# Kernel tuning notes

Hardware: AMD Instinct MI355X
Metric: run time of the kernel (lower is better)

Reference implementation:

```python
import jax, jax.numpy as jnp
import numpy as np

D_MODEL = 1024
NUM_HEADS = 16
HEAD_DIM = D_MODEL // NUM_HEADS


def setup_inputs() -> dict:
    key = jax.random.key(0)
    ks = jax.random.split(key, 9)
    B, S = 4, 2048
    s = 1.0 / np.sqrt(D_MODEL)
    return {
        "x": jax.random.normal(ks[0], (B, S, D_MODEL), dtype=jnp.float32),
        "Wq": jax.random.normal(ks[1], (D_MODEL, D_MODEL), dtype=jnp.float32) * s,
        "bq": jnp.zeros((D_MODEL,), dtype=jnp.float32),
        "Wk": jax.random.normal(ks[2], (D_MODEL, HEAD_DIM), dtype=jnp.float32) * s,
        "bk": jnp.zeros((HEAD_DIM,), dtype=jnp.float32),
        "Wv": jax.random.normal(ks[3], (D_MODEL, HEAD_DIM), dtype=jnp.float32) * s,
        "bv": jnp.zeros((HEAD_DIM,), dtype=jnp.float32),
        "Wo": jax.random.normal(ks[4], (D_MODEL, D_MODEL), dtype=jnp.float32) * s,
        "bo": jnp.zeros((D_MODEL,), dtype=jnp.float32),
    }


def reference(x, Wq, bq, Wk, bk, Wv, bv, Wo, bo):
    B, S, _ = x.shape
    H, Dh = NUM_HEADS, HEAD_DIM
    # projections
    Q = (x @ Wq + bq).reshape(B, S, H, Dh).transpose(0, 2, 1, 3)  # [B,H,S,Dh]
    K = x @ Wk + bk  # [B,S,Dh] (single shared KV head)
    V = x @ Wv + bv  # [B,S,Dh]
    # scores: Q @ K^T, broadcasting the single K head over all query heads
    A = jnp.einsum("bhqd,bkd->bhqk", Q, K)  # [B,H,S,S]
    causal = jnp.tril(jnp.ones((S, S), dtype=bool))
    A = jnp.where(causal, A, -jnp.inf)
    # original divides AFTER masking; -inf stays -inf so math is identical
    P = jax.nn.softmax(A / np.sqrt(Dh).astype(np.float32), axis=-1)
    O = jnp.einsum("bhqk,bkd->bhqd", P, V)  # [B,H,S,Dh]
    O = O.transpose(0, 2, 1, 3).reshape(B, S, H * Dh)
    return O @ Wo + bo
```

## Files before the change

kernel.cpp:

```cpp
#include <hip/hip_runtime.h>
#include <hip/hip_bf16.h>

typedef __bf16 bf16_t;
typedef __bf16 bf16x4 __attribute__((ext_vector_type(4)));
typedef __bf16 bf16x8 __attribute__((ext_vector_type(8)));
typedef float f32x4 __attribute__((ext_vector_type(4)));

#define AS1(p) ((const __attribute__((address_space(1))) void*)(p))
#define AS3(p) ((__attribute__((address_space(3))) void*)(p))

__device__ __forceinline__ f32x4 mfma16(bf16x8 a, bf16x8 b, f32x4 c) {
  return __builtin_amdgcn_mfma_f32_16x16x32_bf16(a, b, c, 0, 0, 0);
}

__global__ void prep(const float* __restrict__ x, const float* __restrict__ Wq,
                     const float* __restrict__ Wk, const float* __restrict__ Wv,
                     const float* __restrict__ Wo, const float* __restrict__ bq,
                     const float* __restrict__ bk, const float* __restrict__ bv,
                     bf16_t* __restrict__ xb, bf16_t* __restrict__ WqT,
                     bf16_t* __restrict__ WkvT, bf16_t* __restrict__ WoT,
                     float* __restrict__ bqkv) {
  const int u = blockIdx.x;
  if (u >= 546) {
    int i = ((u - 546) * 256 + threadIdx.x) * 4;
    float4 v = *(const float4*)(x + i);
    bf16x4 o = {(bf16_t)v.x, (bf16_t)v.y, (bf16_t)v.z, (bf16_t)v.w};
    *(bf16x4*)(xb + i) = o;
    return;
  }
  if (u == 544) {
    int i = threadIdx.x * 4;
    *(float4*)(bqkv + i) = *(const float4*)(bq + i);
    return;
  }
  if (u == 545) {
    if (threadIdx.x < 128)
      bqkv[1024 + threadIdx.x] =
          (threadIdx.x < 64) ? bk[threadIdx.x] : bv[threadIdx.x - 64];
    return;
  }
  const float* W; bf16_t* Wt; int N, bx, by;
  if (u < 256)      { W = Wq; Wt = WqT;              N = 1024; bx = u & 15;         by = u >> 4; }
  else if (u < 272) { W = Wk; Wt = WkvT;             N = 64;   bx = 0;              by = u - 256; }
  else if (u < 288) { W = Wv; Wt = WkvT + 64 * 1024; N = 64;   bx = 0;              by = u - 272; }
  else              { W = Wo; Wt = WoT;              N = 1024; bx = (u - 288) & 15; by = (u - 288) >> 4; }
  __shared__ float t[64][65];
  const int n0 = bx * 64, k0 = by * 64;
  const int tx = threadIdx.x & 63, ty = threadIdx.x >> 6;
#pragma unroll
  for (int i = 0; i < 16; ++i)
    t[ty * 16 + i][tx] = W[(size_t)(k0 + ty * 16 + i) * N + n0 + tx];
  __syncthreads();
#pragma unroll
  for (int i = 0; i < 16; ++i)
    Wt[(size_t)(n0 + ty * 16 + i) * 1024 + k0 + tx] = (bf16_t)t[tx][ty * 16 + i];
}

__global__ __launch_bounds__(256, 2)
void gemm_qkv(const bf16_t* __restrict__ A, const bf16_t* __restrict__ Bt,
              const float* __restrict__ bias, bf16_t* __restrict__ Qb,
              bf16_t* __restrict__ KVb, bf16_t* __restrict__ VtG, int M, int K) {
  __shared__ __align__(16) bf16_t As[128 * 32];
  __shared__ __align__(16) bf16_t Bs[128 * 32];
  const int tid = threadIdx.x;
  const int w = tid >> 6, l = tid & 63;
  const int l15 = l & 15, q = l >> 4;
  const int m0 = blockIdx.y * 128, n0 = blockIdx.x * 128;
  const int mw = (w >> 1) * 64, nw = (w & 1) * 64;
  f32x4 acc[4][4] = {};
  const int kb = (l & 3) * 8;
  int rA[2], rB[2];
#pragma unroll
  for (int i = 0; i < 2; ++i) {
    int row = (i * 4 + w) * 16 + (l >> 2);
    rA[i] = m0 + row;
    rB[i] = n0 + row;
  }
  for (int k0 = 0; k0 < K; k0 += 32) {
#pragma unroll
    for (int i = 0; i < 2; ++i) {
      int sg = i * 4 + w;
      __builtin_amdgcn_global_load_lds(AS1(A + (size_t)rA[i] * K + k0 + kb),
                                       AS3(As + sg * 512), 16, 0, 0);
      __builtin_amdgcn_global_load_lds(AS1(Bt + (size_t)rB[i] * K + k0 + kb),
                                       AS3(Bs + sg * 512), 16, 0, 0);
    }
    __syncthreads();
    bf16x8 af[4], bfr[4];
#pragma unroll
    for (int mi = 0; mi < 4; ++mi)
      af[mi] = *(const bf16x8*)(As + (mw + mi * 16 + l15) * 32 + q * 8);
#pragma unroll
    for (int ni = 0; ni < 4; ++ni)
      bfr[ni] = *(const bf16x8*)(Bs + (nw + ni * 16 + l15) * 32 + q * 8);
#pragma unroll
    for (int mi = 0; mi < 4; ++mi)
#pragma unroll
      for (int ni = 0; ni < 4; ++ni)
        acc[mi][ni] = mfma16(af[mi], bfr[ni], acc[mi][ni]);
    __syncthreads();
  }
#pragma unroll
  for (int ni = 0; ni < 4; ++ni) {
    int col = n0 + nw + ni * 16 + l15;
    float bv = bias[col];
#pragma unroll
    for (int mi = 0; mi < 4; ++mi)
#pragma unroll
      for (int r = 0; r < 4; ++r) {
        int row = m0 + mw + mi * 16 + q * 4 + r;
        bf16_t v = (bf16_t)(acc[mi][ni][r] + bv);
        if (col < 1024) {
          Qb[(size_t)row * 1024 + col] = v;
        } else {
          int c2 = col - 1024;
          KVb[(size_t)row * 128 + c2] = v;
          if (c2 >= 64)
            VtG[(size_t)((row >> 11) * 64 + (c2 - 64)) * 2048 + (row & 2047)] = v;
        }
      }
  }
}

__global__ __launch_bounds__(256, 2)
void gemm_nt_bias_f32(const bf16_t* __restrict__ A, const bf16_t* __restrict__ Bt,
                      const float* __restrict__ bias, float* __restrict__ C,
                      int M, int N, int K) {
  __shared__ __align__(16) bf16_t As[128 * 32];
  __shared__ __align__(16) bf16_t Bs[128 * 32];
  const int tid = threadIdx.x;
  const int w = tid >> 6, l = tid & 63;
  const int l15 = l & 15, q = l >> 4;
  const int m0 = blockIdx.y * 128, n0 = blockIdx.x * 128;
  const int mw = (w >> 1) * 64, nw = (w & 1) * 64;
  f32x4 acc[4][4] = {};
  const int kb = (l & 3) * 8;
  int rA[2], rB[2];
#pragma unroll
  for (int i = 0; i < 2; ++i) {
    int row = (i * 4 + w) * 16 + (l >> 2);
    rA[i] = m0 + row;
    int rb = n0 + row; if (rb >= N) rb = N - 1;
    rB[i] = rb;
  }
  for (int k0 = 0; k0 < K; k0 += 32) {
#pragma unroll
    for (int i = 0; i < 2; ++i) {
      int sg = i * 4 + w;
      __builtin_amdgcn_global_load_lds(AS1(A + (size_t)rA[i] * K + k0 + kb),
                                       AS3(As + sg * 512), 16, 0, 0);
      __builtin_amdgcn_global_load_lds(AS1(Bt + (size_t)rB[i] * K + k0 + kb),
                                       AS3(Bs + sg * 512), 16, 0, 0);
    }
    __syncthreads();
    bf16x8 af[4], bfr[4];
#pragma unroll
    for (int mi = 0; mi < 4; ++mi)
      af[mi] = *(const bf16x8*)(As + (mw + mi * 16 + l15) * 32 + q * 8);
#pragma unroll
    for (int ni = 0; ni < 4; ++ni)
      bfr[ni] = *(const bf16x8*)(Bs + (nw + ni * 16 + l15) * 32 + q * 8);
#pragma unroll
    for (int mi = 0; mi < 4; ++mi)
#pragma unroll
      for (int ni = 0; ni < 4; ++ni)
        acc[mi][ni] = mfma16(af[mi], bfr[ni], acc[mi][ni]);
    __syncthreads();
  }
#pragma unroll
  for (int ni = 0; ni < 4; ++ni) {
    int col = n0 + nw + ni * 16 + l15;
    if (col >= N) continue;
    float bv = bias[col];
#pragma unroll
    for (int mi = 0; mi < 4; ++mi)
#pragma unroll
      for (int r = 0; r < 4; ++r) {
        int row = m0 + mw + mi * 16 + q * 4 + r;
        C[(size_t)row * N + col] = acc[mi][ni][r] + bv;
      }
  }
}

__device__ __forceinline__ void load_q(const bf16_t* __restrict__ Qb, int b, int h,
                                       int qt, int l15, int q,
                                       bf16x8 (&qf0)[4], bf16x8 (&qf1)[4]) {
#pragma unroll
  for (int nq = 0; nq < 4; ++nq) {
    const bf16_t* qp = Qb + (size_t)(b * 2048 + qt * 64 + nq * 16 + l15) * 1024 + h * 64 + q * 8;
    qf0[nq] = *(const bf16x8*)qp;
    qf1[nq] = *(const bf16x8*)(qp + 32);
  }
}

template <bool DIAG>
__device__ __forceinline__ void attn_step(
    const bf16_t* __restrict__ kbase, const bf16_t* __restrict__ vbase, int kt,
    int l15, int q, bf16_t* __restrict__ ps,
    const bf16x8 (&qf0)[4], const bf16x8 (&qf1)[4],
    f32x4 (&o)[4][4], float (&rs)[4]) {
  const float c1 = 0.18033688f;
  const bf16_t* kb = kbase + (size_t)kt * 64 * 128;
  bf16x8 ka0[4], ka1[4];
#pragma unroll
  for (int mk = 0; mk < 4; ++mk) {
    const bf16_t* kr = kb + (mk * 16 + l15) * 128;
    ka0[mk] = *(const bf16x8*)(kr + q * 8);
    ka1[mk] = *(const bf16x8*)(kr + 32 + q * 8);
  }
  bf16x8 va0[4], va1[4];
#pragma unroll
  for (int md = 0; md < 4; ++md) {
    const bf16_t* vr = vbase + (size_t)(md * 16 + l15) * 2048 + kt * 64;
    va0[md] = *(const bf16x8*)(vr + q * 8);
    va1[md] = *(const bf16x8*)(vr + 32 + q * 8);
  }
#pragma unroll
  for (int mh = 0; mh < 2; ++mh) {
    f32x4 s2[2][4];
    __builtin_amdgcn_s_setprio(1);
#pragma unroll
    for (int mk2 = 0; mk2 < 2; ++mk2)
#pragma unroll
      for (int nq = 0; nq < 4; ++nq) {
        f32x4 t = {0.f, 0.f, 0.f, 0.f};
        t = mfma16(ka0[mh * 2 + mk2], qf0[nq], t);
        t = mfma16(ka1[mh * 2 + mk2], qf1[nq], t);
        s2[mk2][nq] = t;
      }
    __builtin_amdgcn_s_setprio(0);
#pragma unroll
    for (int nq = 0; nq < 4; ++nq)
#pragma unroll
      for (int mk2 = 0; mk2 < 2; ++mk2) {
        const int mk = mh * 2 + mk2;
        bf16x4 pk;
#pragma unroll
        for (int r = 0; r < 4; ++r) {
          float pv = __builtin_amdgcn_exp2f(s2[mk2][nq][r] * c1 - 16.0f);
          if (DIAG && (mk * 16 + q * 4 + r) > (nq * 16 + l15)) pv = 0.f;
          rs[nq] += pv;
          pk[r] = (bf16_t)pv;
        }
        *(bf16x4*)(ps + nq * 1152 + l15 * 72 + mk * 16 + q * 4) = pk;
      }
  }
#pragma unroll
  for (int nq = 0; nq < 4; ++nq) {
    bf16x8 pb0 = *(const bf16x8*)(ps + nq * 1152 + l15 * 72 + q * 8);
    bf16x8 pb1 = *(const bf16x8*)(ps + nq * 1152 + l15 * 72 + 32 + q * 8);
    __builtin_amdgcn_s_setprio(1);
#pragma unroll
    for (int md = 0; md < 4; ++md) {
      o[md][nq] = mfma16(va0[md], pb0, o[md][nq]);
      o[md][nq] = mfma16(va1[md], pb1, o[md][nq]);
    }
    __builtin_amdgcn_s_setprio(0);
  }
}

__device__ __forceinline__ void attn_finalize(bf16_t* __restrict__ AO, int b, int h,
                                              int qt, int l15, int q,
                                              f32x4 (&o)[4][4], float (&rs)[4]) {
#pragma unroll
  for (int nq = 0; nq < 4; ++nq) {
    rs[nq] += __shfl_xor(rs[nq], 16);
    rs[nq] += __shfl_xor(rs[nq], 32);
  }
  float inv[4];
#pragma unroll
  for (int nq = 0; nq < 4; ++nq) inv[nq] = 1.f / rs[nq];
#pragma unroll
  for (int md = 0; md < 4; ++md)
#pragma unroll
    for (int nq = 0; nq < 4; ++nq) {
      bf16x4 ov = {(bf16_t)(o[md][nq][0] * inv[nq]), (bf16_t)(o[md][nq][1] * inv[nq]),
                   (bf16_t)(o[md][nq][2] * inv[nq]), (bf16_t)(o[md][nq][3] * inv[nq])};
      *(bf16x4*)(AO + (size_t)(b * 2048 + qt * 64 + nq * 16 + l15) * 1024 +
                 h * 64 + md * 16 + q * 4) = ov;
    }
}

__global__ __launch_bounds__(128, 2)
void mqa_attn9(const bf16_t* __restrict__ Qb, const bf16_t* __restrict__ KVb,
               const bf16_t* __restrict__ VtG, bf16_t* __restrict__ AO) {
  __shared__ __align__(16) bf16_t Ps[2][4][16 * 72];
  __shared__ __align__(16) float Oc[4096];
  __shared__ float RSc[256];
  const int u = blockIdx.x;
  const int b = u & 3;
  const int h = (u >> 2) & 15;
  const int p = (u >> 6) & 15;
  const int w = threadIdx.x >> 6, l = threadIdx.x & 63;
  const int l15 = l & 15, q = l >> 4;
  const int qt_h = 31 - p;
  bf16_t* ps = &Ps[w][0][0];
  const bf16_t* kbase = KVb + (size_t)b * 2048 * 128;
  const bf16_t* vbase = VtG + (size_t)b * 64 * 2048;

  bf16x8 qf0[4], qf1[4];
  f32x4 o[4][4] = {};
  float rs[4] = {0.f, 0.f, 0.f, 0.f};

  if (w == 0) {
    load_q(Qb, b, h, qt_h, l15, q, qf0, qf1);
    const int e = (p == 15) ? 16 : 17;
    for (int kt = 0; kt < e; ++kt)
      attn_step<false>(kbase, vbase, kt, l15, q, ps, qf0, qf1, o, rs);
    if (p == 15)
      attn_step<true>(kbase, vbase, 16, l15, q, ps, qf0, qf1, o, rs);
    __syncthreads();
#pragma unroll
    for (int md = 0; md < 4; ++md)
#pragma unroll
      for (int nq = 0; nq < 4; ++nq)
        o[md][nq] += *(const f32x4*)&Oc[((md * 4 + nq) * 64 + l) * 4];
#pragma unroll
    for (int nq = 0; nq < 4; ++nq) rs[nq] += RSc[l * 4 + nq];
    attn_finalize(AO, b, h, qt_h, l15, q, o, rs);
  } else {
    load_q(Qb, b, h, p, l15, q, qf0, qf1);
    for (int kt = 0; kt < p; ++kt)
      attn_step<false>(kbase, vbase, kt, l15, q, ps, qf0, qf1, o, rs);
    attn_step<true>(kbase, vbase, p, l15, q, ps, qf0, qf1, o, rs);
    attn_finalize(AO, b, h, p, l15, q, o, rs);
#pragma unroll
    for (int md = 0; md < 4; ++md)
#pragma unroll
      for (int nq = 0; nq < 4; ++nq) o[md][nq] = f32x4{0.f, 0.f, 0.f, 0.f};
    rs[0] = rs[1] = rs[2] = rs[3] = 0.f;
    if (p < 15) {
      load_q(Qb, b, h, qt_h, l15, q, qf0, qf1);
      for (int kt = 17; kt < 31 - p; ++kt)
        attn_step<false>(kbase, vbase, kt, l15, q, ps, qf0, qf1, o, rs);
      attn_step<true>(kbase, vbase, 31 - p, l15, q, ps, qf0, qf1, o, rs);
    }
#pragma unroll
    for (int md = 0; md < 4; ++md)
#pragma unroll
      for (int nq = 0; nq < 4; ++nq)
        *(f32x4*)&Oc[((md * 4 + nq) * 64 + l) * 4] = o[md][nq];
#pragma unroll
    for (int nq = 0; nq < 4; ++nq) RSc[l * 4 + nq] = rs[nq];
    __syncthreads();
  }
}

extern "C" void kernel_launch(void* const* d_in, const int* in_sizes, int n_in,
                              void* d_out, int out_size, void* d_ws, size_t ws_size,
                              hipStream_t stream) {
  (void)in_sizes; (void)n_in; (void)out_size; (void)ws_size;
  const int BS = 8192;
  const float* x  = (const float*)d_in[0];
  const float* Wq = (const float*)d_in[1];
  const float* bq = (const float*)d_in[2];
  const float* Wk = (const float*)d_in[3];
  const float* bk = (const float*)d_in[4];
  const float* Wv = (const float*)d_in[5];
  const float* bv = (const float*)d_in[6];
  const float* Wo = (const float*)d_in[7];
  const float* bo = (const float*)d_in[8];
  float* out = (float*)d_out;

  bf16_t* p = (bf16_t*)d_ws;
  bf16_t* WqT  = p; p += 1024 * 1024;
  bf16_t* WkvT = p; p += 128 * 1024;
  bf16_t* WoT  = p; p += 1024 * 1024;
  bf16_t* xb   = p; p += (size_t)BS * 1024;
  bf16_t* Qb   = p; p += (size_t)BS * 1024;
  bf16_t* KVb  = p; p += (size_t)BS * 128;
  bf16_t* VtG  = p; p += (size_t)4 * 64 * 2048;
  float*  bqkv = (float*)p; p += 2304;
  bf16_t* AO  = xb;

  prep<<<dim3(546 + 8192), 256, 0, stream>>>(x, Wq, Wk, Wv, Wo, bq, bk, bv,
                                             xb, WqT, WkvT, WoT, bqkv);

  gemm_qkv<<<dim3(9, BS / 128), 256, 0, stream>>>(xb, WqT, bqkv, Qb, KVb, VtG, BS, 1024);

  mqa_attn9<<<dim3(1024), 128, 0, stream>>>(Qb, KVb, VtG, AO);

  gemm_nt_bias_f32<<<dim3(8, BS / 128), 256, 0, stream>>>(AO, WoT, bo, out, BS, 1024, 1024);
}
```

Before: 237.0 us.

## Split attention KV tiles across four waves per query tile and swap GEMM grid order

The attention kernel changes from two waves handling a paired short and long query tile to four waves per single query tile, each wave taking every fourth KV tile. The partial outputs and row sums are then reduced through shared memory that reuses the P buffer. Launch order is longest tiles first, with twice as many blocks. The two GEMMs also swap grid axes so consecutive blocks walk along M and share the same B (weight) tile. The aim is better load balance and more parallelism in attention, plus better weight reuse in cache for the GEMMs. The cost is extra reduction traffic and synchronisation, and the same K/V data is reloaded by more blocks.

```diff
diff --git a/kernel.cpp b/kernel.cpp
--- a/kernel.cpp
+++ b/kernel.cpp
@@ -65,7 +65,7 @@
   const int tid = threadIdx.x;
   const int w = tid >> 6, l = tid & 63;
   const int l15 = l & 15, q = l >> 4;
-  const int m0 = blockIdx.y * 128, n0 = blockIdx.x * 128;
+  const int m0 = blockIdx.x * 128, n0 = blockIdx.y * 128;
   const int mw = (w >> 1) * 64, nw = (w & 1) * 64;
   f32x4 acc[4][4] = {};
   const int kb = (l & 3) * 8;
@@ -131,7 +131,7 @@
   const int tid = threadIdx.x;
   const int w = tid >> 6, l = tid & 63;
   const int l15 = l & 15, q = l >> 4;
-  const int m0 = blockIdx.y * 128, n0 = blockIdx.x * 128;
+  const int m0 = blockIdx.x * 128, n0 = blockIdx.y * 128;
   const int mw = (w >> 1) * 64, nw = (w & 1) * 64;
   f32x4 acc[4][4] = {};
   const int kb = (l & 3) * 8;
@@ -259,6 +259,29 @@
   }
 }
 
+__device__ __forceinline__ void stash_partial(float* __restrict__ cb, int l,
+                                              const f32x4 (&o)[4][4],
+                                              const float (&rs)[4]) {
+#pragma unroll
+  for (int md = 0; md < 4; ++md)
+#pragma unroll
+    for (int nq = 0; nq < 4; ++nq)
+      *(f32x4*)&cb[((md * 4 + nq) * 64 + l) * 4] = o[md][nq];
+#pragma unroll
+  for (int nq = 0; nq < 4; ++nq) cb[4096 + l * 4 + nq] = rs[nq];
+}
+
+__device__ __forceinline__ void accum_partial(const float* __restrict__ cb, int l,
+                                              f32x4 (&o)[4][4], float (&rs)[4]) {
+#pragma unroll
+  for (int md = 0; md < 4; ++md)
+#pragma unroll
+    for (int nq = 0; nq < 4; ++nq)
+      o[md][nq] += *(const f32x4*)&cb[((md * 4 + nq) * 64 + l) * 4];
+#pragma unroll
+  for (int nq = 0; nq < 4; ++nq) rs[nq] += cb[4096 + l * 4 + nq];
+}
+
 __device__ __forceinline__ void attn_finalize(bf16_t* __restrict__ AO, int b, int h,
                                               int qt, int l15, int q,
                                               f32x4 (&o)[4][4], float (&rs)[4]) {
@@ -281,19 +304,16 @@
     }
 }
 
-__global__ __launch_bounds__(128, 2)
-void mqa_attn9(const bf16_t* __restrict__ Qb, const bf16_t* __restrict__ KVb,
-               const bf16_t* __restrict__ VtG, bf16_t* __restrict__ AO) {
-  __shared__ __align__(16) bf16_t Ps[2][4][16 * 72];
-  __shared__ __align__(16) float Oc[4096];
-  __shared__ float RSc[256];
+__global__ __launch_bounds__(256, 2)
+void mqa_attn12(const bf16_t* __restrict__ Qb, const bf16_t* __restrict__ KVb,
+                const bf16_t* __restrict__ VtG, bf16_t* __restrict__ AO) {
+  __shared__ __align__(16) bf16_t Ps[4][4][16 * 72];
   const int u = blockIdx.x;
   const int b = u & 3;
   const int h = (u >> 2) & 15;
-  const int p = (u >> 6) & 15;
+  const int qt = 31 - (u >> 6);
   const int w = threadIdx.x >> 6, l = threadIdx.x & 63;
   const int l15 = l & 15, q = l >> 4;
-  const int qt_h = 31 - p;
   bf16_t* ps = &Ps[w][0][0];
   const bf16_t* kbase = KVb + (size_t)b * 2048 * 128;
   const bf16_t* vbase = VtG + (size_t)b * 64 * 2048;
@@ -302,47 +322,26 @@
   f32x4 o[4][4] = {};
   float rs[4] = {0.f, 0.f, 0.f, 0.f};
 
+  load_q(Qb, b, h, qt, l15, q, qf0, qf1);
+  for (int kt = w; kt < qt; kt += 4)
+    attn_step<false>(kbase, vbase, kt, l15, q, ps, qf0, qf1, o, rs);
+  if ((qt & 3) == w)
+    attn_step<true>(kbase, vbase, qt, l15, q, ps, qf0, qf1, o, rs);
+
+  float* cbA = (float*)&Ps[0][0][0];
+  float* cbB = (float*)&Ps[2][0][0];
+  __syncthreads();
+  if (w == 1) stash_partial(cbA, l, o, rs);
+  if (w == 3) stash_partial(cbB, l, o, rs);
+  __syncthreads();
+  if (w == 0) accum_partial(cbA, l, o, rs);
+  if (w == 2) accum_partial(cbB, l, o, rs);
+  __syncthreads();
+  if (w == 2) stash_partial(cbA, l, o, rs);
+  __syncthreads();
   if (w == 0) {
-    load_q(Qb, b, h, qt_h, l15, q, qf0, qf1);
-    const int e = (p == 15) ? 16 : 17;
-    for (int kt = 0; kt < e; ++kt)
-      attn_step<false>(kbase, vbase, kt, l15, q, ps, qf0, qf1, o, rs);
-    if (p == 15)
-      attn_step<true>(kbase, vbase, 16, l15, q, ps, qf0, qf1, o, rs);
-    __syncthreads();
-#pragma unroll
-    for (int md = 0; md < 4; ++md)
-#pragma unroll
-      for (int nq = 0; nq < 4; ++nq)
-        o[md][nq] += *(const f32x4*)&Oc[((md * 4 + nq) * 64 + l) * 4];
-#pragma unroll
-    for (int nq = 0; nq < 4; ++nq) rs[nq] += RSc[l * 4 + nq];
-    attn_finalize(AO, b, h, qt_h, l15, q, o, rs);
-  } else {
-    load_q(Qb, b, h, p, l15, q, qf0, qf1);
-    for (int kt = 0; kt < p; ++kt)
-      attn_step<false>(kbase, vbase, kt, l15, q, ps, qf0, qf1, o, rs);
-    attn_step<true>(kbase, vbase, p, l15, q, ps, qf0, qf1, o, rs);
-    attn_finalize(AO, b, h, p, l15, q, o, rs);
-#pragma unroll
-    for (int md = 0; md < 4; ++md)
-#pragma unroll
-      for (int nq = 0; nq < 4; ++nq) o[md][nq] = f32x4{0.f, 0.f, 0.f, 0.f};
-    rs[0] = rs[1] = rs[2] = rs[3] = 0.f;
-    if (p < 15) {
-      load_q(Qb, b, h, qt_h, l15, q, qf0, qf1);
-      for (int kt = 17; kt < 31 - p; ++kt)
-        attn_step<false>(kbase, vbase, kt, l15, q, ps, qf0, qf1, o, rs);
-      attn_step<true>(kbase, vbase, 31 - p, l15, q, ps, qf0, qf1, o, rs);
-    }
-#pragma unroll
-    for (int md = 0; md < 4; ++md)
-#pragma unroll
-      for (int nq = 0; nq < 4; ++nq)
-        *(f32x4*)&Oc[((md * 4 + nq) * 64 + l) * 4] = o[md][nq];
-#pragma unroll
-    for (int nq = 0; nq < 4; ++nq) RSc[l * 4 + nq] = rs[nq];
-    __syncthreads();
+    accum_partial(cbA, l, o, rs);
+    attn_finalize(AO, b, h, qt, l15, q, o, rs);
   }
 }
 
@@ -376,9 +375,9 @@
   prep<<<dim3(546 + 8192), 256, 0, stream>>>(x, Wq, Wk, Wv, Wo, bq, bk, bv,
                                              xb, WqT, WkvT, WoT, bqkv);
 
-  gemm_qkv<<<dim3(9, BS / 128), 256, 0, stream>>>(xb, WqT, bqkv, Qb, KVb, VtG, BS, 1024);
-
-  mqa_attn9<<<dim3(1024), 128, 0, stream>>>(Qb, KVb, VtG, AO);
-
-  gemm_nt_bias_f32<<<dim3(8, BS / 128), 256, 0, stream>>>(AO, WoT, bo, out, BS, 1024, 1024);
-}
+  gemm_qkv<<<dim3(BS / 128, 9), 256, 0, stream>>>(xb, WqT, bqkv, Qb, KVb, VtG, BS, 1024);
+
+  mqa_attn12<<<dim3(2048), 256, 0, stream>>>(Qb, KVb, VtG, AO);
+
+  gemm_nt_bias_f32<<<dim3(BS / 128, 8), 256, 0, stream>>>(AO, WoT, bo, out, BS, 1024, 1024);
+}
```

Result: no change. 232.9 us (-1.7%).
